# Performance work log

Measured on AMD Instinct MI355X. Metric: run time of the kernel, lower is better.

Reference implementation:

```python
import jax, jax.numpy as jnp
import numpy as np

K, M, N = 8, 1024, 1024  # bits, in_features, out_features (nf)
B_, S_ = 4, 2048

def setup_inputs() -> dict:
    key = jax.random.key(0)
    k1, k2, k3, k4 = jax.random.split(key, 4)
    x = jax.random.normal(k1, (B_, S_, M), dtype=jnp.float32)
    # per-bit +/-1 sign matrices, stored as float (module casts int8 -> x.dtype)
    binary = jnp.where(jax.random.normal(k2, (K, M, N)) > 0, 1.0, -1.0).astype(jnp.float32)
    # positive per-bit, per-output-channel scales (sup decomposition yields positives)
    scale = jax.random.uniform(k3, (K, 1, N), dtype=jnp.float32, minval=0.01, maxval=1.0)
    bias = jax.random.normal(k4, (N,), dtype=jnp.float32)
    return {"x": x, "binary": binary, "scale": scale, "bias": bias}

def reference(x, binary, scale, bias):
    size_out = x.shape[:-1] + (N,)
    x2 = x.reshape(-1, x.shape[-1])                 # [T, m]
    # k separate dense matmuls against +/-1 matrices: [k, T, n]
    xk = jnp.einsum('tm,kmn->ktn', x2, binary)
    out = jnp.sum(xk * scale, axis=0)               # per-bit scale then sum over bits
    out = out + bias
    return out.reshape(size_out)
```

## Files before the change

kernel.cpp:

```cpp
#include <hip/hip_runtime.h>
#include <cstdint>

#define TDIM 8192
#define MDIM 1024
#define NDIM 1024
#define KBITS 8
#define BK 64
#define TT 128
#define TN 128

typedef __bf16 bf16x8 __attribute__((ext_vector_type(8)));
typedef float f32x4 __attribute__((ext_vector_type(4)));
typedef float f32x16 __attribute__((ext_vector_type(16)));

#define GAS(p) ((__attribute__((address_space(1))) void*)(uintptr_t)(p))
#define LAS(p) ((__attribute__((address_space(3))) void*)(uintptr_t)(p))

__device__ __forceinline__ unsigned short f2bf(float f) {
    union { float f; unsigned u; } v; v.f = f;
    unsigned r = v.u + 0x7fffu + ((v.u >> 16) & 1u);
    return (unsigned short)(r >> 16);
}

__global__ __launch_bounds__(256) void prep_kernel(const float* __restrict__ x,
                                                   unsigned short* __restrict__ xb,
                                                   const float* __restrict__ binary,
                                                   const float* __restrict__ scale,
                                                   unsigned short* __restrict__ wtr) {
    __shared__ float tile[32][33];
    const int tid = threadIdx.x;
    if (blockIdx.x >= 1024) {
        const int b = blockIdx.x - 1024;
        const int tb = b >> 3;
        const int gchunk = b & 7;
#pragma unroll
        for (int p = 0; p < 2; ++p) {
            const int flat = tid + p * 256;
            const int goff = (flat & 7) | (p << 3);
            const int r = (flat >> 3) & 31;
            const int g = gchunk * 16 + goff;
            const float* src = x + ((size_t)tb * 32 + r) * MDIM + g * 8;
            float4 a = *(const float4*)(src);
            float4 c = *(const float4*)(src + 4);
            uint4 o;
            o.x = (unsigned)f2bf(a.x) | ((unsigned)f2bf(a.y) << 16);
            o.y = (unsigned)f2bf(a.z) | ((unsigned)f2bf(a.w) << 16);
            o.z = (unsigned)f2bf(c.x) | ((unsigned)f2bf(c.y) << 16);
            o.w = (unsigned)f2bf(c.z) | ((unsigned)f2bf(c.w) << 16);
            *(uint4*)(xb + (((size_t)tb * 128 + g) * 32 + r) * 8) = o;
        }
        return;
    }
    const int n0 = (blockIdx.x & 31) * 32;
    const int m0 = (blockIdx.x >> 5) * 32;
    const int r = tid >> 3;
    const int cn = (tid & 7) * 4;
    f32x4 acc = {0.f, 0.f, 0.f, 0.f};
#pragma unroll
    for (int k = 0; k < KBITS; ++k) {
        f32x4 v = *(const f32x4*)(binary + ((size_t)k * MDIM + m0 + r) * NDIM + n0 + cn);
        f32x4 s = *(const f32x4*)(scale + (size_t)k * NDIM + n0 + cn);
        acc += v * s;
    }
#pragma unroll
    for (int e = 0; e < 4; ++e) tile[cn + e][r] = acc[e];
    __syncthreads();
    const int rn = tid >> 3;
    const int cm = (tid & 7) * 4;
    ushort4 o4;
    o4.x = f2bf(tile[rn][cm + 0]);
    o4.y = f2bf(tile[rn][cm + 1]);
    o4.z = f2bf(tile[rn][cm + 2]);
    o4.w = f2bf(tile[rn][cm + 3]);
    *(ushort4*)(wtr + (size_t)(n0 + rn) * MDIM + m0 + cm) = o4;
}

__global__ __launch_bounds__(256) void gemm_kernel(const unsigned short* __restrict__ xb,
                                                   const unsigned short* __restrict__ wtr,
                                                   const float* __restrict__ bias,
                                                   float* __restrict__ out) {
    __shared__ __attribute__((aligned(16))) unsigned short sB[2 * TN * BK];

    const int tid = threadIdx.x;
    const int lane = tid & 63;
    const int wv = tid >> 6;
    const int wrow = wv >> 1;
    const int wcol = wv & 1;
    const int lr = lane & 31;
    const int half = lane >> 5;

    const int t0 = blockIdx.x * TT;
    const int n0 = blockIdx.y * TN;

    const unsigned short* srcB[4];
    unsigned short* dstB[4];
#pragma unroll
    for (int j = 0; j < 4; ++j) {
        int s = tid + j * 256;
        int r = s >> 3;
        int g = (s & 7) ^ (r & 7);
        srcB[j] = wtr + (size_t)(n0 + r) * MDIM + g * 8;
        dstB[j] = sB + s * 8;
    }

    const unsigned short* aptr[2];
#pragma unroll
    for (int i = 0; i < 2; ++i) {
        size_t tb = (size_t)(t0 >> 5) + wrow * 2 + i;
        aptr[i] = xb + (tb * 128 + half) * 256 + lr * 8;
    }

    int b_off[4][2];
#pragma unroll
    for (int c = 0; c < 4; ++c)
#pragma unroll
        for (int j = 0; j < 2; ++j) {
            int n = wcol * 64 + j * 32 + lr;
            b_off[c][j] = (n * 8 + ((2 * c + half) ^ (n & 7))) * 8;
        }

    f32x16 acc[2][2];
#pragma unroll
    for (int i = 0; i < 2; ++i)
#pragma unroll
        for (int j = 0; j < 2; ++j)
#pragma unroll
            for (int r = 0; r < 16; ++r) acc[i][j][r] = 0.f;

#pragma unroll
    for (int j = 0; j < 4; ++j)
        __builtin_amdgcn_global_load_lds(GAS(srcB[j]), LAS(dstB[j]), 16, 0, 0);
    __syncthreads();

    for (int it = 0; it < MDIM / BK; ++it) {
        const int buf = (it & 1) << 13;
        if (it < MDIM / BK - 1) {
            const int nbuf = 8192 - buf;
            const int kof = (it + 1) * BK;
#pragma unroll
            for (int j = 0; j < 4; ++j)
                __builtin_amdgcn_global_load_lds(GAS(srcB[j] + kof), LAS(dstB[j] + nbuf), 16, 0, 0);
        }
        const int aof = it * (BK * 32);
#pragma unroll
        for (int c = 0; c < 4; ++c) {
            bf16x8 a0 = *(const bf16x8*)(aptr[0] + aof + c * 512);
            bf16x8 a1 = *(const bf16x8*)(aptr[1] + aof + c * 512);
            bf16x8 b0 = *(const bf16x8*)(sB + buf + b_off[c][0]);
            bf16x8 b1 = *(const bf16x8*)(sB + buf + b_off[c][1]);
            acc[0][0] = __builtin_amdgcn_mfma_f32_32x32x16_bf16(a0, b0, acc[0][0], 0, 0, 0);
            acc[1][0] = __builtin_amdgcn_mfma_f32_32x32x16_bf16(a1, b0, acc[1][0], 0, 0, 0);
            acc[0][1] = __builtin_amdgcn_mfma_f32_32x32x16_bf16(a0, b1, acc[0][1], 0, 0, 0);
            acc[1][1] = __builtin_amdgcn_mfma_f32_32x32x16_bf16(a1, b1, acc[1][1], 0, 0, 0);
        }
        __syncthreads();
    }

#pragma unroll
    for (int j = 0; j < 2; ++j) {
        const int n = n0 + wcol * 64 + j * 32 + lr;
        const float bv = bias[n];
#pragma unroll
        for (int i = 0; i < 2; ++i) {
            const int tb = t0 + wrow * 64 + i * 32;
#pragma unroll
            for (int r = 0; r < 16; ++r) {
                const int t = tb + (r & 3) + 8 * (r >> 2) + 4 * half;
                out[(size_t)t * NDIM + n] = acc[i][j][r] + bv;
            }
        }
    }
}

extern "C" void kernel_launch(void* const* d_in, const int* in_sizes, int n_in,
                              void* d_out, int out_size, void* d_ws, size_t ws_size,
                              hipStream_t stream) {
    const float* x      = (const float*)d_in[0];
    const float* binary = (const float*)d_in[1];
    const float* scale  = (const float*)d_in[2];
    const float* bias   = (const float*)d_in[3];
    float* out = (float*)d_out;

    unsigned short* xb  = (unsigned short*)d_ws;
    unsigned short* wtr = xb + (size_t)TDIM * MDIM;

    prep_kernel<<<1024 + 2048, 256, 0, stream>>>(x, xb, binary, scale, wtr);
    gemm_kernel<<<dim3(TDIM / TT, NDIM / TN), 256, 0, stream>>>(xb, wtr, bias, out);
}
```

Measured before the change: 127.2 us.

## Halve GEMM token tile, raise occupancy, and prefetch A fragments across iterations

Result: no change. 128.5 us (+1.0%).

```diff
diff --git a/kernel.cpp b/kernel.cpp
--- a/kernel.cpp
+++ b/kernel.cpp
@@ -6,8 +6,9 @@
 #define NDIM 1024
 #define KBITS 8
 #define BK 64
-#define TT 128
+#define TT 64
 #define TN 128
+#define NITER (MDIM / BK)
 
 typedef __bf16 bf16x8 __attribute__((ext_vector_type(8)));
 typedef float f32x4 __attribute__((ext_vector_type(4)));
@@ -75,10 +76,10 @@
     *(ushort4*)(wtr + (size_t)(n0 + rn) * MDIM + m0 + cm) = o4;
 }
 
-__global__ __launch_bounds__(256) void gemm_kernel(const unsigned short* __restrict__ xb,
-                                                   const unsigned short* __restrict__ wtr,
-                                                   const float* __restrict__ bias,
-                                                   float* __restrict__ out) {
+__global__ __launch_bounds__(256, 4) void gemm_kernel(const unsigned short* __restrict__ xb,
+                                                      const unsigned short* __restrict__ wtr,
+                                                      const float* __restrict__ bias,
+                                                      float* __restrict__ out) {
     __shared__ __attribute__((aligned(16))) unsigned short sB[2 * TN * BK];
 
     const int tid = threadIdx.x;
@@ -103,12 +104,8 @@
         dstB[j] = sB + s * 8;
     }
 
-    const unsigned short* aptr[2];
-#pragma unroll
-    for (int i = 0; i < 2; ++i) {
-        size_t tb = (size_t)(t0 >> 5) + wrow * 2 + i;
-        aptr[i] = xb + (tb * 128 + half) * 256 + lr * 8;
-    }
+    const size_t tb = (size_t)(t0 >> 5) + wrow;
+    const unsigned short* aBase = xb + tb * 32768 + (size_t)lr * 8;
 
     int b_off[4][2];
 #pragma unroll
@@ -119,41 +116,43 @@
             b_off[c][j] = (n * 8 + ((2 * c + half) ^ (n & 7))) * 8;
         }
 
-    f32x16 acc[2][2];
+    f32x16 acc[2];
 #pragma unroll
-    for (int i = 0; i < 2; ++i)
+    for (int j = 0; j < 2; ++j)
 #pragma unroll
-        for (int j = 0; j < 2; ++j)
-#pragma unroll
-            for (int r = 0; r < 16; ++r) acc[i][j][r] = 0.f;
+        for (int r = 0; r < 16; ++r) acc[j][r] = 0.f;
 
 #pragma unroll
     for (int j = 0; j < 4; ++j)
         __builtin_amdgcn_global_load_lds(GAS(srcB[j]), LAS(dstB[j]), 16, 0, 0);
+    bf16x8 acur[4], anext[4];
+#pragma unroll
+    for (int c = 0; c < 4; ++c)
+        acur[c] = *(const bf16x8*)(aBase + (size_t)(2 * c + half) * 256);
     __syncthreads();
 
-    for (int it = 0; it < MDIM / BK; ++it) {
+    for (int it = 0; it < NITER; ++it) {
         const int buf = (it & 1) << 13;
-        if (it < MDIM / BK - 1) {
+        if (it + 1 < NITER) {
             const int nbuf = 8192 - buf;
             const int kof = (it + 1) * BK;
 #pragma unroll
             for (int j = 0; j < 4; ++j)
                 __builtin_amdgcn_global_load_lds(GAS(srcB[j] + kof), LAS(dstB[j] + nbuf), 16, 0, 0);
+#pragma unroll
+            for (int c = 0; c < 4; ++c)
+                anext[c] = *(const bf16x8*)(aBase + (size_t)((it + 1) * 8 + 2 * c + half) * 256);
         }
-        const int aof = it * (BK * 32);
 #pragma unroll
         for (int c = 0; c < 4; ++c) {
-            bf16x8 a0 = *(const bf16x8*)(aptr[0] + aof + c * 512);
-            bf16x8 a1 = *(const bf16x8*)(aptr[1] + aof + c * 512);
             bf16x8 b0 = *(const bf16x8*)(sB + buf + b_off[c][0]);
             bf16x8 b1 = *(const bf16x8*)(sB + buf + b_off[c][1]);
-            acc[0][0] = __builtin_amdgcn_mfma_f32_32x32x16_bf16(a0, b0, acc[0][0], 0, 0, 0);
-            acc[1][0] = __builtin_amdgcn_mfma_f32_32x32x16_bf16(a1, b0, acc[1][0], 0, 0, 0);
-            acc[0][1] = __builtin_amdgcn_mfma_f32_32x32x16_bf16(a0, b1, acc[0][1], 0, 0, 0);
-            acc[1][1] = __builtin_amdgcn_mfma_f32_32x32x16_bf16(a1, b1, acc[1][1], 0, 0, 0);
+            acc[0] = __builtin_amdgcn_mfma_f32_32x32x16_bf16(acur[c], b0, acc[0], 0, 0, 0);
+            acc[1] = __builtin_amdgcn_mfma_f32_32x32x16_bf16(acur[c], b1, acc[1], 0, 0, 0);
         }
         __syncthreads();
+#pragma unroll
+        for (int c = 0; c < 4; ++c) acur[c] = anext[c];
     }
 
 #pragma unroll
@@ -161,13 +160,9 @@
         const int n = n0 + wcol * 64 + j * 32 + lr;
         const float bv = bias[n];
 #pragma unroll
-        for (int i = 0; i < 2; ++i) {
-            const int tb = t0 + wrow * 64 + i * 32;
-#pragma unroll
-            for (int r = 0; r < 16; ++r) {
-                const int t = tb + (r & 3) + 8 * (r >> 2) + 4 * half;
-                out[(size_t)t * NDIM + n] = acc[i][j][r] + bv;
-            }
+        for (int r = 0; r < 16; ++r) {
+            const int t = t0 + wrow * 32 + (r & 3) + 8 * (r >> 2) + 4 * half;
+            out[(size_t)t * NDIM + n] = acc[j][r] + bv;
         }
     }
 }
```
